# Performance work log

Measured on AMD Instinct MI355X. Metric: run time of the kernel, lower is better.

## Reference

```python
import jax, jax.numpy as jnp
import numpy as np

B, S, D, H = 2, 2048, 1024, 16
HD = D // H  # head_dim = 64
ROPE_BASE = 10000.0


def _rope_cos_sin(seq_len, head_dim, dtype=jnp.float32):
    inv_freq = 1.0 / (ROPE_BASE ** (jnp.arange(0, head_dim, 2, dtype=jnp.float32) / head_dim))
    t = jnp.arange(seq_len, dtype=jnp.float32)
    freqs = jnp.einsum('i,j->ij', t, inv_freq)          # [S, HD/2]
    emb = jnp.concatenate([freqs, freqs], axis=-1)       # [S, HD]
    return jnp.cos(emb).astype(dtype), jnp.sin(emb).astype(dtype)


def _rotate_half(x):
    x1, x2 = jnp.split(x, 2, axis=-1)
    return jnp.concatenate([-x2, x1], axis=-1)


def setup_inputs() -> dict:
    key = jax.random.key(0)
    ks = jax.random.split(key, 5)
    scale = 1.0 / np.sqrt(D)
    return {
        'hidden_states': jax.random.normal(ks[0], (B, S, D), dtype=jnp.float32),
        'Wq': jax.random.normal(ks[1], (D, D), dtype=jnp.float32) * scale,
        'Wk': jax.random.normal(ks[2], (D, D), dtype=jnp.float32) * scale,
        'Wv': jax.random.normal(ks[3], (D, D), dtype=jnp.float32) * scale,
        'Wo': jax.random.normal(ks[4], (D, D), dtype=jnp.float32) * scale,
    }


def reference(hidden_states, Wq, Wk, Wv, Wo):
    b, s, d = hidden_states.shape
    # torch nn.Linear(weight W) computes x @ W^T
    q = hidden_states @ Wq.T
    k = hidden_states @ Wk.T
    v = hidden_states @ Wv.T
    # [B, H, S, HD]
    q = q.reshape(b, s, H, HD).transpose(0, 2, 1, 3)
    k = k.reshape(b, s, H, HD).transpose(0, 2, 1, 3)
    v = v.reshape(b, s, H, HD).transpose(0, 2, 1, 3)
    cos, sin = _rope_cos_sin(s, HD, q.dtype)  # [S, HD]
    cos = cos[None, None]  # [1,1,S,HD]
    sin = sin[None, None]
    q = q * cos + _rotate_half(q) * sin
    k = k * cos + _rotate_half(k) * sin
    scale = HD ** -0.5
    attn = jnp.einsum('bhqd,bhkd->bhqk', q, k) * scale
    attn = jax.nn.softmax(attn.astype(jnp.float32), axis=-1).astype(q.dtype)
    out = jnp.einsum('bhqk,bhkd->bhqd', attn, v)
    out = out.transpose(0, 2, 1, 3).reshape(b, s, d)
    return out @ Wo.T
```

## Files before the change

kernel.cpp:

```cpp
#include <hip/hip_runtime.h>
#include <math.h>

constexpr int Bc = 2;
constexpr int Sc = 2048;
constexpr int Dc = 1024;
constexpr int Hc = 16;
constexpr int HDc = 64;

constexpr float QSC = 0.125f * 1.4426950408889634f;

typedef __attribute__((ext_vector_type(8))) short bf16x8;
typedef __attribute__((ext_vector_type(4))) float f32x4;
typedef __attribute__((ext_vector_type(4))) unsigned short us4;
typedef __attribute__((ext_vector_type(2))) unsigned int u32x2;
typedef __attribute__((ext_vector_type(4))) unsigned int u32x4;

__device__ __forceinline__ unsigned f2bf(float x) {
    unsigned u = __float_as_uint(x);
    return (u + 0x7FFFu + ((u >> 16) & 1u)) >> 16;
}

__device__ __forceinline__ void split2(float x, unsigned short& h, unsigned short& l) {
    unsigned hh = f2bf(x);
    h = (unsigned short)hh;
    l = (unsigned short)f2bf(x - __uint_as_float(hh << 16));
}

#if __has_builtin(__builtin_amdgcn_permlane32_swap)
__device__ __forceinline__ void plswap32(unsigned& a, unsigned& b) {
    u32x2 r = __builtin_amdgcn_permlane32_swap(a, b, false, false);
    a = r.x; b = r.y;
}
#else
__device__ __forceinline__ void plswap32(unsigned& a, unsigned& b) {
    asm volatile("v_permlane32_swap_b32 %0, %1" : "+v"(a), "+v"(b));
}
#endif
#if __has_builtin(__builtin_amdgcn_permlane16_swap)
__device__ __forceinline__ void plswap16(unsigned& a, unsigned& b) {
    u32x2 r = __builtin_amdgcn_permlane16_swap(a, b, false, false);
    a = r.x; b = r.y;
}
#else
__device__ __forceinline__ void plswap16(unsigned& a, unsigned& b) {
    asm volatile("v_permlane16_swap_b32 %0, %1" : "+v"(a), "+v"(b));
}
#endif

__device__ __forceinline__ void exppack(const f32x4& sv, unsigned& w0, unsigned& w1) {
    unsigned u0 = __float_as_uint(__builtin_amdgcn_exp2f(sv[0]));
    unsigned u1 = __float_as_uint(__builtin_amdgcn_exp2f(sv[1]));
    unsigned u2 = __float_as_uint(__builtin_amdgcn_exp2f(sv[2]));
    unsigned u3 = __float_as_uint(__builtin_amdgcn_exp2f(sv[3]));
    w0 = __builtin_amdgcn_perm(u1, u0, 0x07060302u);
    w1 = __builtin_amdgcn_perm(u3, u2, 0x07060302u);
}

__global__ void rope_table(float* __restrict__ ct, float* __restrict__ st_) {
    int id = blockIdx.x * 256 + threadIdx.x;
    int s = id >> 5;
    int i = id & 31;
    double invf = pow(10000.0, -(double)i / 32.0);
    double ang = (double)s * invf;
    ct[id] = (float)cos(ang);
    st_[id] = (float)sin(ang);
}

__global__ void split_xw(const float* __restrict__ x,
                         const float* __restrict__ Wq, const float* __restrict__ Wk,
                         const float* __restrict__ Wv, const float* __restrict__ Wo,
                         unsigned short* __restrict__ xh,
                         unsigned short* __restrict__ whAll, unsigned short* __restrict__ wlAll) {
    int y = blockIdx.y;
    const float* src;
    unsigned short* h;
    unsigned short* l = nullptr;
    int n;
    if (y == 0) { src = x; h = xh; n = 1 << 22; }
    else {
        src = (y == 1) ? Wq : (y == 2) ? Wk : (y == 3) ? Wv : Wo;
        h = whAll + (size_t)(y - 1) * (1 << 20);
        if (y == 4) l = wlAll + (size_t)3 * (1 << 20);
        n = 1 << 20;
    }
    int i = (blockIdx.x * 256 + threadIdx.x) * 4;
    if (i >= n) return;
    float4 v = *(const float4*)(src + i);
    us4 hh;
    ((unsigned short*)&hh)[0] = (unsigned short)f2bf(v.x);
    ((unsigned short*)&hh)[1] = (unsigned short)f2bf(v.y);
    ((unsigned short*)&hh)[2] = (unsigned short)f2bf(v.z);
    ((unsigned short*)&hh)[3] = (unsigned short)f2bf(v.w);
    *(us4*)(h + i) = hh;
    if (l) {
        us4 ll;
        const float* vp = (const float*)&v;
#pragma unroll
        for (int e = 0; e < 4; e++) {
            unsigned short hi = ((unsigned short*)&hh)[e];
            ((unsigned short*)&ll)[e] =
                (unsigned short)f2bf(vp[e] - __uint_as_float((unsigned)hi << 16));
        }
        *(us4*)(l + i) = ll;
    }
}

__global__ __launch_bounds__(512, 4) void gemm_qkv(
    const unsigned short* __restrict__ Ah,
    const unsigned short* __restrict__ whAll,
    unsigned short* __restrict__ Qh,
    unsigned short* __restrict__ Kh,
    unsigned short* __restrict__ Vh,
    const float* __restrict__ ct, const float* __restrict__ st_) {
    constexpr int K = 1024;
    __shared__ __align__(16) unsigned short As[2 * 4096], Bs[2 * 4096];

    const int z = blockIdx.z;
    const unsigned short* Wh = whAll + (size_t)z * (1 << 20);

    const int t = threadIdx.x;
    const int lane = t & 63;
    const int wave = t >> 6;
    const int l = lane & 15;
    const int quad = lane >> 4;
    const int wr = wave >> 1;
    const int wc = wave & 1;
    const int m0 = blockIdx.x * 128;
    const int n0 = blockIdx.y * 128;

    const int arow = t & 127, akc = t >> 7;
    const unsigned short* gA = Ah + (size_t)(m0 + arow) * K + akc * 8;
    const unsigned short* gB = Wh + (size_t)(n0 + arow) * K + akc * 8;

    f32x4 acc[2][4];
#pragma unroll
    for (int i = 0; i < 2; i++)
#pragma unroll
        for (int j = 0; j < 4; j++) acc[i][j] = (f32x4){0.f, 0.f, 0.f, 0.f};

    __builtin_amdgcn_global_load_lds(
        (const __attribute__((address_space(1))) unsigned int*)gA,
        (__attribute__((address_space(3))) unsigned int*)(As + t * 8), 16, 0, 0);
    __builtin_amdgcn_global_load_lds(
        (const __attribute__((address_space(1))) unsigned int*)gB,
        (__attribute__((address_space(3))) unsigned int*)(Bs + t * 8), 16, 0, 0);

    for (int it = 0; it < 32; ++it) {
        __syncthreads();
        if (it + 1 < 32) {
            const int koff = (it + 1) * 32;
            const int bo = ((it + 1) & 1) * 4096;
            __builtin_amdgcn_global_load_lds(
                (const __attribute__((address_space(1))) unsigned int*)(gA + koff),
                (__attribute__((address_space(3))) unsigned int*)(As + bo + t * 8), 16, 0, 0);
            __builtin_amdgcn_global_load_lds(
                (const __attribute__((address_space(1))) unsigned int*)(gB + koff),
                (__attribute__((address_space(3))) unsigned int*)(Bs + bo + t * 8), 16, 0, 0);
        }
        const unsigned short* a = As + (it & 1) * 4096;
        const unsigned short* bb = Bs + (it & 1) * 4096;
        bf16x8 ah[2], bh[4];
#pragma unroll
        for (int i = 0; i < 2; i++)
            ah[i] = *(const bf16x8*)&a[(quad * 128 + wr * 32 + i * 16 + l) * 8];
#pragma unroll
        for (int j = 0; j < 4; j++)
            bh[j] = *(const bf16x8*)&bb[(quad * 128 + wc * 64 + j * 16 + l) * 8];
#pragma unroll
        for (int i = 0; i < 2; i++)
#pragma unroll
            for (int j = 0; j < 4; j++)
                acc[i][j] = __builtin_amdgcn_mfma_f32_16x16x32_bf16(ah[i], bh[j], acc[i][j], 0, 0, 0);
    }

    const int hcol = blockIdx.y * 2 + wc;
    if (z == 2) {
#pragma unroll
        for (int i = 0; i < 2; i++) {
            int m_base = m0 + wr * 32 + i * 16 + quad * 4;
            int bbk = m_base >> 11;
            int T = (m_base & (Sc - 1)) >> 6;
            int ii = (2 * wr + i) & 3;
            int kk = ii >> 1;
            int qd = ((ii & 1) << 1) | (quad >> 1);
            int tj = (quad & 1) * 4;
            size_t tilebase = (((size_t)(bbk * Hc + hcol)) * 32 + T) * 4096;
#pragma unroll
            for (int jj = 0; jj < 4; jj++) {
                int d = jj * 16 + l;
                size_t off = tilebase + (size_t)(((kk * 4 + qd) * 64 + d) * 8 + tj);
                us4 v4;
#pragma unroll
                for (int r = 0; r < 4; r++)
                    ((unsigned short*)&v4)[r] = (unsigned short)f2bf(acc[i][jj][r]);
                *(us4*)(Vh + off) = v4;
            }
        }
    } else {
#pragma unroll
        for (int i = 0; i < 2; i++)
#pragma unroll
            for (int r = 0; r < 4; r++) {
                int m = m0 + wr * 32 + i * 16 + quad * 4 + r;
                int bbk = m >> 11, s = m & (Sc - 1);
#pragma unroll
                for (int jp = 0; jp < 2; jp++) {
                    int d = jp * 16 + l;
                    float cs = ct[s * 32 + d];
                    float sn = st_[s * 32 + d];
                    float x0 = acc[i][jp][r];
                    float x1 = acc[i][jp + 2][r];
                    float y0 = x0 * cs - x1 * sn;
                    float y1 = x1 * cs + x0 * sn;
                    if (z == 0) {
                        size_t rowb = (((size_t)(bbk * Hc + hcol)) * Sc + s) * HDc;
                        Qh[rowb + d]      = (unsigned short)f2bf(y0 * QSC);
                        Qh[rowb + d + 32] = (unsigned short)f2bf(y1 * QSC);
                    } else {
                        int T = s >> 6, tok = s & 63;
                        size_t tb = (((size_t)(bbk * Hc + hcol)) * 32 + T) * 8;
                        size_t off0 = ((tb + (d >> 3)) * 64 + tok) * 8 + (d & 7);
                        size_t off1 = ((tb + (d >> 3) + 4) * 64 + tok) * 8 + (d & 7);
                        Kh[off0] = (unsigned short)f2bf(y0);
                        Kh[off1] = (unsigned short)f2bf(y1);
                    }
                }
            }
    }
}

__global__ __launch_bounds__(512) void attn10(
    const unsigned short* __restrict__ Qh,
    const unsigned short* __restrict__ Kh,
    const unsigned short* __restrict__ Vh,
    unsigned short* __restrict__ AOh, unsigned short* __restrict__ AOl) {
    __shared__ __align__(16) unsigned short KsH[3 * 4096], VtH[3 * 4096];

    const int t = threadIdx.x;
    const int lane = t & 63;
    const int wave = t >> 6;
    const int l = lane & 15;
    const int quad = lane >> 4;
    const int id = blockIdx.x;
    const int bh = (id & 7) * 4 + (id >> 6);
    const int qt = (id >> 3) & 7;
    const int q0 = qt * 256;
    const int b = bh >> 4;
    const int hh = bh & 15;

    const bf16x8 ONES8 = {(short)0x3F80, (short)0x3F80, (short)0x3F80, (short)0x3F80,
                          (short)0x3F80, (short)0x3F80, (short)0x3F80, (short)0x3F80};

    bf16x8 qf[2][2];
#pragma unroll
    for (int bnd = 0; bnd < 2; bnd++) {
        size_t rowb = ((size_t)bh * Sc + q0 + wave * 32 + bnd * 16 + l) * HDc;
#pragma unroll
        for (int ks = 0; ks < 2; ks++)
            qf[bnd][ks] = *(const bf16x8*)(Qh + rowb + ks * 32 + quad * 8);
    }

    f32x4 o[2][4], lac[2];
#pragma unroll
    for (int bnd = 0; bnd < 2; bnd++) {
        lac[bnd] = (f32x4){0.f, 0.f, 0.f, 0.f};
#pragma unroll
        for (int i = 0; i < 4; i++) o[bnd][i] = (f32x4){0.f, 0.f, 0.f, 0.f};
    }

    const int tensor = wave >> 2;
    const int coff0 = (wave * 2) & 7;
    unsigned short* larr = tensor ? VtH : KsH;
    const unsigned short* gT =
        (tensor ? Vh : Kh) + (size_t)bh * Sc * HDc + coff0 * 512 + lane * 8;

#pragma unroll
    for (int q = 0; q < 2; q++)
        __builtin_amdgcn_global_load_lds(
            (const __attribute__((address_space(1))) unsigned int*)(gT + q * 512),
            (__attribute__((address_space(3))) unsigned int*)(larr + coff0 * 512 + q * 512),
            16, 0, 0);

    int bc = 0;
    for (int kt = 0; kt < 32; kt++) {
        if (kt + 1 < 32) {
            int nb = bc + 1; if (nb == 3) nb = 0;
            const unsigned short* g = gT + (size_t)(kt + 1) * 4096;
            unsigned short* dst = larr + nb * 4096 + coff0 * 512;
#pragma unroll
            for (int q = 0; q < 2; q++)
                __builtin_amdgcn_global_load_lds(
                    (const __attribute__((address_space(1))) unsigned int*)(g + q * 512),
                    (__attribute__((address_space(3))) unsigned int*)(dst + q * 512),
                    16, 0, 0);
            asm volatile("s_waitcnt vmcnt(2)" ::: "memory");
        } else {
            asm volatile("s_waitcnt vmcnt(0)" ::: "memory");
        }
        __builtin_amdgcn_s_barrier();
        const unsigned short* Kbuf = KsH + bc * 4096;
        const unsigned short* Vbuf = VtH + bc * 4096;

        f32x4 s[2][4];
#pragma unroll
        for (int bnd = 0; bnd < 2; bnd++)
#pragma unroll
            for (int tt = 0; tt < 4; tt++) s[bnd][tt] = (f32x4){0.f, 0.f, 0.f, 0.f};
        __builtin_amdgcn_s_setprio(1);
#pragma unroll
        for (int ks = 0; ks < 2; ks++)
#pragma unroll
            for (int tt = 0; tt < 4; tt++) {
                bf16x8 kf = *(const bf16x8*)&Kbuf[((ks * 4 + quad) * 64 + tt * 16 + l) * 8];
                s[0][tt] = __builtin_amdgcn_mfma_f32_16x16x32_bf16(kf, qf[0][ks], s[0][tt], 0, 0, 0);
                s[1][tt] = __builtin_amdgcn_mfma_f32_16x16x32_bf16(kf, qf[1][ks], s[1][tt], 0, 0, 0);
            }
        __builtin_amdgcn_s_setprio(0);

        bf16x8 pf[2][2];
#pragma unroll
        for (int bnd = 0; bnd < 2; bnd++)
#pragma unroll
            for (int ttp = 0; ttp < 2; ttp++) {
                unsigned A0, A1, B0, B1;
                exppack(s[bnd][2 * ttp], A0, A1);
                exppack(s[bnd][2 * ttp + 1], B0, B1);
                plswap32(A0, B0);
                plswap16(A0, B0);
                plswap32(A1, B1);
                plswap16(A1, B1);
                u32x4 fw = {A0, A1, B0, B1};
                bf16x8 p8 = __builtin_bit_cast(bf16x8, fw);
                pf[bnd][ttp] = p8;
                lac[bnd] = __builtin_amdgcn_mfma_f32_16x16x32_bf16(ONES8, p8, lac[bnd], 0, 0, 0);
            }

        __builtin_amdgcn_s_setprio(1);
#pragma unroll
        for (int kk = 0; kk < 2; kk++)
#pragma unroll
            for (int dd = 0; dd < 4; dd++) {
                bf16x8 vf = *(const bf16x8*)
                    &Vbuf[(size_t)((kk * 4 + quad) * 64 + dd * 16 + l) * 8];
                o[0][dd] = __builtin_amdgcn_mfma_f32_16x16x32_bf16(vf, pf[0][kk], o[0][dd], 0, 0, 0);
                o[1][dd] = __builtin_amdgcn_mfma_f32_16x16x32_bf16(vf, pf[1][kk], o[1][dd], 0, 0, 0);
            }
        __builtin_amdgcn_s_setprio(0);
        if (++bc == 3) bc = 0;
    }

#pragma unroll
    for (int bnd = 0; bnd < 2; bnd++) {
        float inv = 1.f / lac[bnd][0];
        int q = q0 + wave * 32 + bnd * 16 + l;
        size_t rowb = ((size_t)b * Sc + q) * Dc + hh * HDc + quad * 4;
#pragma unroll
        for (int dd = 0; dd < 4; dd++) {
            us4 h4, l4;
#pragma unroll
            for (int r = 0; r < 4; r++)
                split2(o[bnd][dd][r] * inv,
                       ((unsigned short*)&h4)[r], ((unsigned short*)&l4)[r]);
            *(us4*)(AOh + rowb + dd * 16) = h4;
            *(us4*)(AOl + rowb + dd * 16) = l4;
        }
    }
}

__global__ __launch_bounds__(512, 4) void gemm_out(
    const unsigned short* __restrict__ Ah, const unsigned short* __restrict__ Al,
    const unsigned short* __restrict__ Wh, const unsigned short* __restrict__ Wl,
    float* __restrict__ C0, float* __restrict__ C1) {
    constexpr int K = 1024;
    __shared__ __align__(16) unsigned short AsH[2 * 4096], AsL[2 * 4096],
                                            BsH[2 * 4096], BsL[2 * 4096];

    const int t = threadIdx.x;
    const int lane = t & 63;
    const int wave = t >> 6;
    const int l = lane & 15;
    const int quad = lane >> 4;
    const int wr = wave >> 1;
    const int wc = wave & 1;
    const int m0 = blockIdx.x * 128;
    const int n0 = blockIdx.y * 128;
    const int k0 = blockIdx.z * 512;
    float* __restrict__ C = blockIdx.z ? C1 : C0;

    const int arow = t & 127, akc = t >> 7;
    const unsigned short* gah = Ah + (size_t)(m0 + arow) * K + k0 + akc * 8;
    const unsigned short* gal = Al + (size_t)(m0 + arow) * K + k0 + akc * 8;
    const unsigned short* gbh = Wh + (size_t)(n0 + arow) * K + k0 + akc * 8;
    const unsigned short* gbl = Wl + (size_t)(n0 + arow) * K + k0 + akc * 8;

    f32x4 acc[2][4];
#pragma unroll
    for (int i = 0; i < 2; i++)
#pragma unroll
        for (int j = 0; j < 4; j++) acc[i][j] = (f32x4){0.f, 0.f, 0.f, 0.f};

#define STAGE_OUT(koff, bo)                                                                \
    do {                                                                                   \
        __builtin_amdgcn_global_load_lds(                                                  \
            (const __attribute__((address_space(1))) unsigned int*)(gah + (koff)),         \
            (__attribute__((address_space(3))) unsigned int*)(AsH + (bo) + t * 8), 16, 0, 0); \
        __builtin_amdgcn_global_load_lds(                                                  \
            (const __attribute__((address_space(1))) unsigned int*)(gal + (koff)),         \
            (__attribute__((address_space(3))) unsigned int*)(AsL + (bo) + t * 8), 16, 0, 0); \
        __builtin_amdgcn_global_load_lds(                                                  \
            (const __attribute__((address_space(1))) unsigned int*)(gbh + (koff)),         \
            (__attribute__((address_space(3))) unsigned int*)(BsH + (bo) + t * 8), 16, 0, 0); \
        __builtin_amdgcn_global_load_lds(                                                  \
            (const __attribute__((address_space(1))) unsigned int*)(gbl + (koff)),         \
            (__attribute__((address_space(3))) unsigned int*)(BsL + (bo) + t * 8), 16, 0, 0); \
    } while (0)

    STAGE_OUT(0, 0);

    for (int it = 0; it < 16; ++it) {
        __syncthreads();
        if (it + 1 < 16) STAGE_OUT((it + 1) * 32, ((it + 1) & 1) * 4096);
        const int bo = (it & 1) * 4096;
        bf16x8 ah[2], al[2], bh[4], bl[4];
#pragma unroll
        for (int i = 0; i < 2; i++) {
            int ra = bo + (quad * 128 + wr * 32 + i * 16 + l) * 8;
            ah[i] = *(const bf16x8*)&AsH[ra];
            al[i] = *(const bf16x8*)&AsL[ra];
        }
#pragma unroll
        for (int j = 0; j < 4; j++) {
            int rb = bo + (quad * 128 + wc * 64 + j * 16 + l) * 8;
            bh[j] = *(const bf16x8*)&BsH[rb];
            bl[j] = *(const bf16x8*)&BsL[rb];
        }
#pragma unroll
        for (int i = 0; i < 2; i++)
#pragma unroll
            for (int j = 0; j < 4; j++) {
                acc[i][j] = __builtin_amdgcn_mfma_f32_16x16x32_bf16(ah[i], bh[j], acc[i][j], 0, 0, 0);
                acc[i][j] = __builtin_amdgcn_mfma_f32_16x16x32_bf16(al[i], bh[j], acc[i][j], 0, 0, 0);
                acc[i][j] = __builtin_amdgcn_mfma_f32_16x16x32_bf16(ah[i], bl[j], acc[i][j], 0, 0, 0);
            }
    }
#undef STAGE_OUT

#pragma unroll
    for (int i = 0; i < 2; i++)
#pragma unroll
        for (int j = 0; j < 4; j++)
#pragma unroll
            for (int r = 0; r < 4; r++) {
                int m = m0 + wr * 32 + i * 16 + quad * 4 + r;
                int n = n0 + wc * 64 + j * 16 + l;
                C[(size_t)m * Dc + n] = acc[i][j][r];
            }
}

__global__ void add_partial(float* __restrict__ out, const float* __restrict__ p1) {
    int i = (blockIdx.x * 256 + threadIdx.x) * 4;
    float4 a = *(const float4*)(out + i);
    float4 b = *(const float4*)(p1 + i);
    a.x += b.x; a.y += b.y; a.z += b.z; a.w += b.w;
    *(float4*)(out + i) = a;
}

extern "C" void kernel_launch(void* const* d_in, const int* in_sizes, int n_in,
                              void* d_out, int out_size, void* d_ws, size_t ws_size,
                              hipStream_t stream) {
    const float* x  = (const float*)d_in[0];
    const float* Wq = (const float*)d_in[1];
    const float* Wk = (const float*)d_in[2];
    const float* Wv = (const float*)d_in[3];
    const float* Wo = (const float*)d_in[4];
    float* out = (float*)d_out;

    unsigned short* usw = (unsigned short*)d_ws;
    const size_t M4 = (size_t)1 << 22;
    unsigned short* whAll = usw;
    unsigned short* wlAll = usw + M4;
    unsigned short* xh = usw + 2 * M4;
    unsigned short* xl = usw + 3 * M4;
    unsigned short* Qh = usw + 4 * M4;
    unsigned short* Kh = usw + 5 * M4;
    unsigned short* Vh = usw + 6 * M4;
    float* ct = (float*)(usw + 7 * M4);
    float* st_ = ct + (size_t)Sc * 32;
    unsigned short* AOh = xh;
    unsigned short* AOl = xl;
    float* P1 = (float*)Qh;

    rope_table<<<dim3((Sc * 32) / 256), dim3(256), 0, stream>>>(ct, st_);
    split_xw<<<dim3(4096, 5), dim3(256), 0, stream>>>(x, Wq, Wk, Wv, Wo, xh, whAll, wlAll);
    gemm_qkv<<<dim3(32, 8, 3), dim3(512), 0, stream>>>(
        xh, whAll, Qh, Kh, Vh, ct, st_);
    attn10<<<dim3(256), dim3(512), 0, stream>>>(Qh, Kh, Vh, AOh, AOl);
    gemm_out<<<dim3(32, 8, 2), dim3(512), 0, stream>>>(
        AOh, AOl, whAll + 3 * (1 << 20), wlAll + 3 * (1 << 20), out, P1);
    add_partial<<<dim3(4096), dim3(256), 0, stream>>>(out, P1);
}
```

Baseline: 229.4 us.

## Enlarge QKV GEMM tiles to 256x256 with finer-grained staged pipeline

Result: slower. 241.7 us (+5.4%).

```diff
diff --git a/kernel.cpp b/kernel.cpp
--- a/kernel.cpp
+++ b/kernel.cpp
@@ -14,6 +14,9 @@
 typedef __attribute__((ext_vector_type(4))) unsigned short us4;
 typedef __attribute__((ext_vector_type(2))) unsigned int u32x2;
 typedef __attribute__((ext_vector_type(4))) unsigned int u32x4;
+
+typedef const __attribute__((address_space(1))) unsigned int* gp_t;
+typedef __attribute__((address_space(3))) unsigned int* lp_t;
 
 __device__ __forceinline__ unsigned f2bf(float x) {
     unsigned u = __float_as_uint(x);
@@ -105,7 +108,7 @@
     }
 }
 
-__global__ __launch_bounds__(512, 4) void gemm_qkv(
+__global__ __launch_bounds__(512, 2) void gemm_qkv8(
     const unsigned short* __restrict__ Ah,
     const unsigned short* __restrict__ whAll,
     unsigned short* __restrict__ Qh,
@@ -113,81 +116,122 @@
     unsigned short* __restrict__ Vh,
     const float* __restrict__ ct, const float* __restrict__ st_) {
     constexpr int K = 1024;
-    __shared__ __align__(16) unsigned short As[2 * 4096], Bs[2 * 4096];
-
-    const int z = blockIdx.z;
-    const unsigned short* Wh = whAll + (size_t)z * (1 << 20);
+    __shared__ __align__(16) unsigned short As[2][16384], Bs[2][16384];
 
     const int t = threadIdx.x;
     const int lane = t & 63;
     const int wave = t >> 6;
-    const int l = lane & 15;
+    const int l15 = lane & 15;
     const int quad = lane >> 4;
-    const int wr = wave >> 1;
-    const int wc = wave & 1;
-    const int m0 = blockIdx.x * 128;
-    const int n0 = blockIdx.y * 128;
-
-    const int arow = t & 127, akc = t >> 7;
-    const unsigned short* gA = Ah + (size_t)(m0 + arow) * K + akc * 8;
-    const unsigned short* gB = Wh + (size_t)(n0 + arow) * K + akc * 8;
-
-    f32x4 acc[2][4];
-#pragma unroll
-    for (int i = 0; i < 2; i++)
+    const int wr = wave >> 2;
+    const int wc = wave & 3;
+    const int m0 = blockIdx.x * 256;
+    const int n0 = blockIdx.y * 256;
+    const int z = blockIdx.z;
+    const unsigned short* Wh = whAll + (size_t)z * (1 << 20);
+
+    const int kcr0 = (2 * wave + 0) >> 2, rb0 = ((2 * wave + 0) & 3) * 64;
+    const int kcr1 = (2 * wave + 1) >> 2, rb1 = ((2 * wave + 1) & 3) * 64;
+    const unsigned short* gA0 = Ah + (size_t)(m0 + rb0 + lane) * K + kcr0 * 8;
+    const unsigned short* gA1 = Ah + (size_t)(m0 + rb1 + lane) * K + kcr1 * 8;
+    const unsigned short* gB0 = Wh + (size_t)(n0 + rb0 + lane) * K + kcr0 * 8;
+    const unsigned short* gB1 = Wh + (size_t)(n0 + rb1 + lane) * K + kcr1 * 8;
+    const int ld0 = (kcr0 * 256 + rb0 + lane) * 8;
+    const int ld1 = (kcr1 * 256 + rb1 + lane) * 8;
+
+    f32x4 acc[8][4];
+#pragma unroll
+    for (int i = 0; i < 8; i++)
 #pragma unroll
         for (int j = 0; j < 4; j++) acc[i][j] = (f32x4){0.f, 0.f, 0.f, 0.f};
-
-    __builtin_amdgcn_global_load_lds(
-        (const __attribute__((address_space(1))) unsigned int*)gA,
-        (__attribute__((address_space(3))) unsigned int*)(As + t * 8), 16, 0, 0);
-    __builtin_amdgcn_global_load_lds(
-        (const __attribute__((address_space(1))) unsigned int*)gB,
-        (__attribute__((address_space(3))) unsigned int*)(Bs + t * 8), 16, 0, 0);
-
-    for (int it = 0; it < 32; ++it) {
-        __syncthreads();
-        if (it + 1 < 32) {
-            const int koff = (it + 1) * 32;
-            const int bo = ((it + 1) & 1) * 4096;
-            __builtin_amdgcn_global_load_lds(
-                (const __attribute__((address_space(1))) unsigned int*)(gA + koff),
-                (__attribute__((address_space(3))) unsigned int*)(As + bo + t * 8), 16, 0, 0);
-            __builtin_amdgcn_global_load_lds(
-                (const __attribute__((address_space(1))) unsigned int*)(gB + koff),
-                (__attribute__((address_space(3))) unsigned int*)(Bs + bo + t * 8), 16, 0, 0);
-        }
-        const unsigned short* a = As + (it & 1) * 4096;
-        const unsigned short* bb = Bs + (it & 1) * 4096;
-        bf16x8 ah[2], bh[4];
-#pragma unroll
-        for (int i = 0; i < 2; i++)
-            ah[i] = *(const bf16x8*)&a[(quad * 128 + wr * 32 + i * 16 + l) * 8];
-#pragma unroll
-        for (int j = 0; j < 4; j++)
-            bh[j] = *(const bf16x8*)&bb[(quad * 128 + wc * 64 + j * 16 + l) * 8];
-#pragma unroll
-        for (int i = 0; i < 2; i++)
-#pragma unroll
-            for (int j = 0; j < 4; j++)
-                acc[i][j] = __builtin_amdgcn_mfma_f32_16x16x32_bf16(ah[i], bh[j], acc[i][j], 0, 0, 0);
-    }
-
-    const int hcol = blockIdx.y * 2 + wc;
+    bf16x8 af[8];
+
+#define STG(g0, g1, LARR, X, KH) do {                                                      \
+        const int _ko = (X) * 64 + (KH) * 32;                                              \
+        const int _lo = (KH) * 8192;                                                       \
+        __builtin_amdgcn_global_load_lds((gp_t)((g0) + _ko),                               \
+            (lp_t)(&LARR[(X) & 1][ld0 + _lo]), 16, 0, 0);                                  \
+        __builtin_amdgcn_global_load_lds((gp_t)((g1) + _ko),                               \
+            (lp_t)(&LARR[(X) & 1][ld1 + _lo]), 16, 0, 0);                                  \
+    } while (0)
+
+#define VM10 asm volatile("s_waitcnt vmcnt(10)" ::: "memory")
+#define VM8  asm volatile("s_waitcnt vmcnt(8)" ::: "memory")
+#define VM4  asm volatile("s_waitcnt vmcnt(4)" ::: "memory")
+#define VM0  asm volatile("s_waitcnt vmcnt(0)" ::: "memory")
+
+#define CPH(BUF, KS, J0, RA, PRE) do {                                                     \
+        PRE;                                                                               \
+        asm volatile("s_barrier" ::: "memory");                                            \
+        const unsigned short* _a = &As[(BUF)][0];                                          \
+        const unsigned short* _b = &Bs[(BUF)][0];                                          \
+        if (RA) {                                                                          \
+            _Pragma("unroll")                                                              \
+            for (int _i = 0; _i < 8; _i++)                                                 \
+                af[_i] = *(const bf16x8*)&_a[((KS) * 4 + quad) * 2048 +                    \
+                                             (wr * 128 + _i * 16 + l15) * 8];              \
+        }                                                                                  \
+        bf16x8 _bf0 = *(const bf16x8*)&_b[((KS) * 4 + quad) * 2048 +                       \
+                                          (wc * 64 + (J0) * 16 + l15) * 8];                \
+        bf16x8 _bf1 = *(const bf16x8*)&_b[((KS) * 4 + quad) * 2048 +                       \
+                                          (wc * 64 + ((J0) + 1) * 16 + l15) * 8];          \
+        __builtin_amdgcn_s_setprio(1);                                                     \
+        _Pragma("unroll")                                                                  \
+        for (int _i = 0; _i < 8; _i++) {                                                   \
+            acc[_i][(J0)]     = __builtin_amdgcn_mfma_f32_16x16x32_bf16(af[_i], _bf0,      \
+                                    acc[_i][(J0)], 0, 0, 0);                               \
+            acc[_i][(J0) + 1] = __builtin_amdgcn_mfma_f32_16x16x32_bf16(af[_i], _bf1,      \
+                                    acc[_i][(J0) + 1], 0, 0, 0);                           \
+        }                                                                                  \
+        __builtin_amdgcn_s_setprio(0);                                                     \
+        asm volatile("s_barrier" ::: "memory");                                            \
+    } while (0)
+
+    STG(gA0, gA1, As, 0, 0); STG(gB0, gB1, Bs, 0, 0);
+    STG(gA0, gA1, As, 0, 1); STG(gB0, gB1, Bs, 0, 1);
+    STG(gA0, gA1, As, 1, 0); STG(gB0, gB1, Bs, 1, 0);
+
+    for (int e = 0; e < 14; e += 2) {
+        CPH(0, 0, 0, 1, STG(gA0, gA1, As, e + 1, 1); VM10);
+        CPH(0, 0, 2, 0, STG(gB0, gB1, Bs, e + 1, 1));
+        CPH(0, 1, 0, 1, STG(gA0, gA1, As, e + 2, 0); VM10);
+        CPH(0, 1, 2, 0, STG(gB0, gB1, Bs, e + 2, 0));
+        CPH(1, 0, 0, 1, STG(gA0, gA1, As, e + 2, 1); VM10);
+        CPH(1, 0, 2, 0, STG(gB0, gB1, Bs, e + 2, 1));
+        CPH(1, 1, 0, 1, STG(gA0, gA1, As, e + 3, 0); VM10);
+        CPH(1, 1, 2, 0, STG(gB0, gB1, Bs, e + 3, 0));
+    }
+    CPH(0, 0, 0, 1, STG(gA0, gA1, As, 15, 1); VM10);
+    CPH(0, 0, 2, 0, STG(gB0, gB1, Bs, 15, 1));
+    CPH(0, 1, 0, 1, VM8);
+    CPH(0, 1, 2, 0, );
+    CPH(1, 0, 0, 1, VM4);
+    CPH(1, 0, 2, 0, );
+    CPH(1, 1, 0, 1, VM0);
+    CPH(1, 1, 2, 0, );
+
+#undef CPH
+#undef STG
+#undef VM10
+#undef VM8
+#undef VM4
+#undef VM0
+
+    const int hcol = blockIdx.y * 4 + wc;
     if (z == 2) {
 #pragma unroll
-        for (int i = 0; i < 2; i++) {
-            int m_base = m0 + wr * 32 + i * 16 + quad * 4;
+        for (int i = 0; i < 8; i++) {
+            int m_base = m0 + wr * 128 + i * 16 + quad * 4;
             int bbk = m_base >> 11;
             int T = (m_base & (Sc - 1)) >> 6;
-            int ii = (2 * wr + i) & 3;
+            int ii = i & 3;
             int kk = ii >> 1;
             int qd = ((ii & 1) << 1) | (quad >> 1);
             int tj = (quad & 1) * 4;
             size_t tilebase = (((size_t)(bbk * Hc + hcol)) * 32 + T) * 4096;
 #pragma unroll
             for (int jj = 0; jj < 4; jj++) {
-                int d = jj * 16 + l;
+                int d = jj * 16 + l15;
                 size_t off = tilebase + (size_t)(((kk * 4 + qd) * 64 + d) * 8 + tj);
                 us4 v4;
 #pragma unroll
@@ -198,14 +242,14 @@
         }
     } else {
 #pragma unroll
-        for (int i = 0; i < 2; i++)
+        for (int i = 0; i < 8; i++)
 #pragma unroll
             for (int r = 0; r < 4; r++) {
-                int m = m0 + wr * 32 + i * 16 + quad * 4 + r;
+                int m = m0 + wr * 128 + i * 16 + quad * 4 + r;
                 int bbk = m >> 11, s = m & (Sc - 1);
 #pragma unroll
                 for (int jp = 0; jp < 2; jp++) {
-                    int d = jp * 16 + l;
+                    int d = jp * 16 + l15;
                     float cs = ct[s * 32 + d];
                     float sn = st_[s * 32 + d];
                     float x0 = acc[i][jp][r];
@@ -277,8 +321,8 @@
 #pragma unroll
     for (int q = 0; q < 2; q++)
         __builtin_amdgcn_global_load_lds(
-            (const __attribute__((address_space(1))) unsigned int*)(gT + q * 512),
-            (__attribute__((address_space(3))) unsigned int*)(larr + coff0 * 512 + q * 512),
+            (gp_t)(gT + q * 512),
+            (lp_t)(larr + coff0 * 512 + q * 512),
             16, 0, 0);
 
     int bc = 0;
@@ -290,8 +334,8 @@
 #pragma unroll
             for (int q = 0; q < 2; q++)
                 __builtin_amdgcn_global_load_lds(
-                    (const __attribute__((address_space(1))) unsigned int*)(g + q * 512),
-                    (__attribute__((address_space(3))) unsigned int*)(dst + q * 512),
+                    (gp_t)(g + q * 512),
+                    (lp_t)(dst + q * 512),
                     16, 0, 0);
             asm volatile("s_waitcnt vmcnt(2)" ::: "memory");
         } else {
@@ -401,18 +445,14 @@
 
 #define STAGE_OUT(koff, bo)                                                                \
     do {                                                                                   \
-        __builtin_amdgcn_global_load_lds(                                                  \
-            (const __attribute__((address_space(1))) unsigned int*)(gah + (koff)),         \
-            (__attribute__((address_space(3))) unsigned int*)(AsH + (bo) + t * 8), 16, 0, 0); \
-        __builtin_amdgcn_global_load_lds(                                                  \
-            (const __attribute__((address_space(1))) unsigned int*)(gal + (koff)),         \
-            (__attribute__((address_space(3))) unsigned int*)(AsL + (bo) + t * 8), 16, 0, 0); \
-        __builtin_amdgcn_global_load_lds(                                                  \
-            (const __attribute__((address_space(1))) unsigned int*)(gbh + (koff)),         \
-            (__attribute__((address_space(3))) unsigned int*)(BsH + (bo) + t * 8), 16, 0, 0); \
-        __builtin_amdgcn_global_load_lds(                                                  \
-            (const __attribute__((address_space(1))) unsigned int*)(gbl + (koff)),         \
-            (__attribute__((address_space(3))) unsigned int*)(BsL + (bo) + t * 8), 16, 0, 0); \
+        __builtin_amdgcn_global_load_lds((gp_t)(gah + (koff)),                             \
+            (lp_t)(AsH + (bo) + t * 8), 16, 0, 0);                                         \
+        __builtin_amdgcn_global_load_lds((gp_t)(gal + (koff)),                             \
+            (lp_t)(AsL + (bo) + t * 8), 16, 0, 0);                                         \
+        __builtin_amdgcn_global_load_lds((gp_t)(gbh + (koff)),                             \
+            (lp_t)(BsH + (bo) + t * 8), 16, 0, 0);                                         \
+        __builtin_amdgcn_global_load_lds((gp_t)(gbl + (koff)),                             \
+            (lp_t)(BsL + (bo) + t * 8), 16, 0, 0);                                         \
     } while (0)
 
     STAGE_OUT(0, 0);
@@ -492,7 +532,7 @@
 
     rope_table<<<dim3((Sc * 32) / 256), dim3(256), 0, stream>>>(ct, st_);
     split_xw<<<dim3(4096, 5), dim3(256), 0, stream>>>(x, Wq, Wk, Wv, Wo, xh, whAll, wlAll);
-    gemm_qkv<<<dim3(32, 8, 3), dim3(512), 0, stream>>>(
+    gemm_qkv8<<<dim3(16, 4, 3), dim3(512), 0, stream>>>(
         xh, whAll, Qh, Kh, Vh, ct, st_);
     attn10<<<dim3(256), dim3(512), 0, stream>>>(Qh, Kh, Vh, AOh, AOl);
     gemm_out<<<dim3(32, 8, 2), dim3(512), 0, stream>>>(
```

## Use row-major XOR-swizzled LDS tiles and K=64 stages in QKV and output GEMMs

Applied to the files above, without the earlier changes.

Result: faster. 203.4 us (-11.4%).

```diff
diff --git a/kernel.cpp b/kernel.cpp
--- a/kernel.cpp
+++ b/kernel.cpp
@@ -14,6 +14,9 @@
 typedef __attribute__((ext_vector_type(4))) unsigned short us4;
 typedef __attribute__((ext_vector_type(2))) unsigned int u32x2;
 typedef __attribute__((ext_vector_type(4))) unsigned int u32x4;
+
+typedef const __attribute__((address_space(1))) unsigned int* gp_t;
+typedef __attribute__((address_space(3))) unsigned int* lp_t;
 
 __device__ __forceinline__ unsigned f2bf(float x) {
     unsigned u = __float_as_uint(x);
@@ -105,7 +108,7 @@
     }
 }
 
-__global__ __launch_bounds__(512, 4) void gemm_qkv(
+__global__ __launch_bounds__(512, 4) void gemm_qkv9(
     const unsigned short* __restrict__ Ah,
     const unsigned short* __restrict__ whAll,
     unsigned short* __restrict__ Qh,
@@ -113,24 +116,27 @@
     unsigned short* __restrict__ Vh,
     const float* __restrict__ ct, const float* __restrict__ st_) {
     constexpr int K = 1024;
-    __shared__ __align__(16) unsigned short As[2 * 4096], Bs[2 * 4096];
-
-    const int z = blockIdx.z;
-    const unsigned short* Wh = whAll + (size_t)z * (1 << 20);
+    __shared__ __align__(16) unsigned short As[2][8192], Bs[2][8192];
 
     const int t = threadIdx.x;
     const int lane = t & 63;
     const int wave = t >> 6;
-    const int l = lane & 15;
+    const int l15 = lane & 15;
     const int quad = lane >> 4;
     const int wr = wave >> 1;
     const int wc = wave & 1;
     const int m0 = blockIdx.x * 128;
     const int n0 = blockIdx.y * 128;
-
-    const int arow = t & 127, akc = t >> 7;
-    const unsigned short* gA = Ah + (size_t)(m0 + arow) * K + akc * 8;
-    const unsigned short* gB = Wh + (size_t)(n0 + arow) * K + akc * 8;
+    const int z = blockIdx.z;
+    const unsigned short* Wh = whAll + (size_t)z * (1 << 20);
+
+    const int c0 = t,        r0 = c0 >> 3, s0 = c0 & 7;
+    const int c1 = t + 512,  r1 = c1 >> 3, s1 = c1 & 7;
+    const unsigned short* gA0 = Ah + (size_t)(m0 + r0) * K + (s0 ^ (r0 & 7)) * 8;
+    const unsigned short* gA1 = Ah + (size_t)(m0 + r1) * K + (s1 ^ (r1 & 7)) * 8;
+    const unsigned short* gB0 = Wh + (size_t)(n0 + r0) * K + (s0 ^ (r0 & 7)) * 8;
+    const unsigned short* gB1 = Wh + (size_t)(n0 + r1) * K + (s1 ^ (r1 & 7)) * 8;
+    const int d0 = c0 * 8, d1 = c1 * 8;
 
     f32x4 acc[2][4];
 #pragma unroll
@@ -138,40 +144,43 @@
 #pragma unroll
         for (int j = 0; j < 4; j++) acc[i][j] = (f32x4){0.f, 0.f, 0.f, 0.f};
 
-    __builtin_amdgcn_global_load_lds(
-        (const __attribute__((address_space(1))) unsigned int*)gA,
-        (__attribute__((address_space(3))) unsigned int*)(As + t * 8), 16, 0, 0);
-    __builtin_amdgcn_global_load_lds(
-        (const __attribute__((address_space(1))) unsigned int*)gB,
-        (__attribute__((address_space(3))) unsigned int*)(Bs + t * 8), 16, 0, 0);
-
-    for (int it = 0; it < 32; ++it) {
+#define STGQ(X) do {                                                                       \
+        const int _ko = (X) * 64;                                                          \
+        const int _bf = (X) & 1;                                                           \
+        __builtin_amdgcn_global_load_lds((gp_t)(gA0 + _ko), (lp_t)(&As[_bf][d0]), 16, 0, 0); \
+        __builtin_amdgcn_global_load_lds((gp_t)(gA1 + _ko), (lp_t)(&As[_bf][d1]), 16, 0, 0); \
+        __builtin_amdgcn_global_load_lds((gp_t)(gB0 + _ko), (lp_t)(&Bs[_bf][d0]), 16, 0, 0); \
+        __builtin_amdgcn_global_load_lds((gp_t)(gB1 + _ko), (lp_t)(&Bs[_bf][d1]), 16, 0, 0); \
+    } while (0)
+
+    STGQ(0);
+
+    for (int it = 0; it < 16; ++it) {
         __syncthreads();
-        if (it + 1 < 32) {
-            const int koff = (it + 1) * 32;
-            const int bo = ((it + 1) & 1) * 4096;
-            __builtin_amdgcn_global_load_lds(
-                (const __attribute__((address_space(1))) unsigned int*)(gA + koff),
-                (__attribute__((address_space(3))) unsigned int*)(As + bo + t * 8), 16, 0, 0);
-            __builtin_amdgcn_global_load_lds(
-                (const __attribute__((address_space(1))) unsigned int*)(gB + koff),
-                (__attribute__((address_space(3))) unsigned int*)(Bs + bo + t * 8), 16, 0, 0);
-        }
-        const unsigned short* a = As + (it & 1) * 4096;
-        const unsigned short* bb = Bs + (it & 1) * 4096;
-        bf16x8 ah[2], bh[4];
-#pragma unroll
-        for (int i = 0; i < 2; i++)
-            ah[i] = *(const bf16x8*)&a[(quad * 128 + wr * 32 + i * 16 + l) * 8];
-#pragma unroll
-        for (int j = 0; j < 4; j++)
-            bh[j] = *(const bf16x8*)&bb[(quad * 128 + wc * 64 + j * 16 + l) * 8];
-#pragma unroll
-        for (int i = 0; i < 2; i++)
-#pragma unroll
-            for (int j = 0; j < 4; j++)
-                acc[i][j] = __builtin_amdgcn_mfma_f32_16x16x32_bf16(ah[i], bh[j], acc[i][j], 0, 0, 0);
-    }
+        if (it + 1 < 16) STGQ(it + 1);
+        const unsigned short* a = &As[it & 1][0];
+        const unsigned short* bb = &Bs[it & 1][0];
+#pragma unroll
+        for (int ks = 0; ks < 2; ks++) {
+            bf16x8 ah[2], bh[4];
+#pragma unroll
+            for (int i = 0; i < 2; i++) {
+                int row = wr * 32 + i * 16 + l15;
+                ah[i] = *(const bf16x8*)&a[row * 64 + ((ks * 4 + quad) ^ (row & 7)) * 8];
+            }
+#pragma unroll
+            for (int j = 0; j < 4; j++) {
+                int row = wc * 64 + j * 16 + l15;
+                bh[j] = *(const bf16x8*)&bb[row * 64 + ((ks * 4 + quad) ^ (row & 7)) * 8];
+            }
+#pragma unroll
+            for (int i = 0; i < 2; i++)
+#pragma unroll
+                for (int j = 0; j < 4; j++)
+                    acc[i][j] = __builtin_amdgcn_mfma_f32_16x16x32_bf16(ah[i], bh[j], acc[i][j], 0, 0, 0);
+        }
+    }
+#undef STGQ
 
     const int hcol = blockIdx.y * 2 + wc;
     if (z == 2) {
@@ -187,7 +196,7 @@
             size_t tilebase = (((size_t)(bbk * Hc + hcol)) * 32 + T) * 4096;
 #pragma unroll
             for (int jj = 0; jj < 4; jj++) {
-                int d = jj * 16 + l;
+                int d = jj * 16 + l15;
                 size_t off = tilebase + (size_t)(((kk * 4 + qd) * 64 + d) * 8 + tj);
                 us4 v4;
 #pragma unroll
@@ -205,7 +214,7 @@
                 int bbk = m >> 11, s = m & (Sc - 1);
 #pragma unroll
                 for (int jp = 0; jp < 2; jp++) {
-                    int d = jp * 16 + l;
+                    int d = jp * 16 + l15;
                     float cs = ct[s * 32 + d];
                     float sn = st_[s * 32 + d];
                     float x0 = acc[i][jp][r];
@@ -277,8 +286,8 @@
 #pragma unroll
     for (int q = 0; q < 2; q++)
         __builtin_amdgcn_global_load_lds(
-            (const __attribute__((address_space(1))) unsigned int*)(gT + q * 512),
-            (__attribute__((address_space(3))) unsigned int*)(larr + coff0 * 512 + q * 512),
+            (gp_t)(gT + q * 512),
+            (lp_t)(larr + coff0 * 512 + q * 512),
             16, 0, 0);
 
     int bc = 0;
@@ -290,8 +299,8 @@
 #pragma unroll
             for (int q = 0; q < 2; q++)
                 __builtin_amdgcn_global_load_lds(
-                    (const __attribute__((address_space(1))) unsigned int*)(g + q * 512),
-                    (__attribute__((address_space(3))) unsigned int*)(dst + q * 512),
+                    (gp_t)(g + q * 512),
+                    (lp_t)(dst + q * 512),
                     16, 0, 0);
             asm volatile("s_waitcnt vmcnt(2)" ::: "memory");
         } else {
@@ -367,18 +376,18 @@
     }
 }
 
-__global__ __launch_bounds__(512, 4) void gemm_out(
+__global__ __launch_bounds__(512, 4) void gemm_out9(
     const unsigned short* __restrict__ Ah, const unsigned short* __restrict__ Al,
     const unsigned short* __restrict__ Wh, const unsigned short* __restrict__ Wl,
     float* __restrict__ C0, float* __restrict__ C1) {
     constexpr int K = 1024;
-    __shared__ __align__(16) unsigned short AsH[2 * 4096], AsL[2 * 4096],
-                                            BsH[2 * 4096], BsL[2 * 4096];
+    __shared__ __align__(16) unsigned short AsH[2][4096], AsL[2][4096],
+                                            BsH[2][4096], BsL[2][4096];
 
     const int t = threadIdx.x;
     const int lane = t & 63;
     const int wave = t >> 6;
-    const int l = lane & 15;
+    const int l15 = lane & 15;
     const int quad = lane >> 4;
     const int wr = wave >> 1;
     const int wc = wave & 1;
@@ -387,11 +396,13 @@
     const int k0 = blockIdx.z * 512;
     float* __restrict__ C = blockIdx.z ? C1 : C0;
 
-    const int arow = t & 127, akc = t >> 7;
-    const unsigned short* gah = Ah + (size_t)(m0 + arow) * K + k0 + akc * 8;
-    const unsigned short* gal = Al + (size_t)(m0 + arow) * K + k0 + akc * 8;
-    const unsigned short* gbh = Wh + (size_t)(n0 + arow) * K + k0 + akc * 8;
-    const unsigned short* gbl = Wl + (size_t)(n0 + arow) * K + k0 + akc * 8;
+    const int rr = t >> 2, ss = t & 3;
+    const int gc = (ss ^ (rr & 3)) * 8;
+    const unsigned short* gah = Ah + (size_t)(m0 + rr) * K + k0 + gc;
+    const unsigned short* gal = Al + (size_t)(m0 + rr) * K + k0 + gc;
+    const unsigned short* gbh = Wh + (size_t)(n0 + rr) * K + k0 + gc;
+    const unsigned short* gbl = Wl + (size_t)(n0 + rr) * K + k0 + gc;
+    const int dd_ = t * 8;
 
     f32x4 acc[2][4];
 #pragma unroll
@@ -399,40 +410,35 @@
 #pragma unroll
         for (int j = 0; j < 4; j++) acc[i][j] = (f32x4){0.f, 0.f, 0.f, 0.f};
 
-#define STAGE_OUT(koff, bo)                                                                \
-    do {                                                                                   \
-        __builtin_amdgcn_global_load_lds(                                                  \
-            (const __attribute__((address_space(1))) unsigned int*)(gah + (koff)),         \
-            (__attribute__((address_space(3))) unsigned int*)(AsH + (bo) + t * 8), 16, 0, 0); \
-        __builtin_amdgcn_global_load_lds(                                                  \
-            (const __attribute__((address_space(1))) unsigned int*)(gal + (koff)),         \
-            (__attribute__((address_space(3))) unsigned int*)(AsL + (bo) + t * 8), 16, 0, 0); \
-        __builtin_amdgcn_global_load_lds(                                                  \
-            (const __attribute__((address_space(1))) unsigned int*)(gbh + (koff)),         \
-            (__attribute__((address_space(3))) unsigned int*)(BsH + (bo) + t * 8), 16, 0, 0); \
-        __builtin_amdgcn_global_load_lds(                                                  \
-            (const __attribute__((address_space(1))) unsigned int*)(gbl + (koff)),         \
-            (__attribute__((address_space(3))) unsigned int*)(BsL + (bo) + t * 8), 16, 0, 0); \
+#define STGO(X) do {                                                                       \
+        const int _ko = (X) * 32;                                                          \
+        const int _bf = (X) & 1;                                                           \
+        __builtin_amdgcn_global_load_lds((gp_t)(gah + _ko), (lp_t)(&AsH[_bf][dd_]), 16, 0, 0); \
+        __builtin_amdgcn_global_load_lds((gp_t)(gal + _ko), (lp_t)(&AsL[_bf][dd_]), 16, 0, 0); \
+        __builtin_amdgcn_global_load_lds((gp_t)(gbh + _ko), (lp_t)(&BsH[_bf][dd_]), 16, 0, 0); \
+        __builtin_amdgcn_global_load_lds((gp_t)(gbl + _ko), (lp_t)(&BsL[_bf][dd_]), 16, 0, 0); \
     } while (0)
 
-    STAGE_OUT(0, 0);
+    STGO(0);
 
     for (int it = 0; it < 16; ++it) {
         __syncthreads();
-        if (it + 1 < 16) STAGE_OUT((it + 1) * 32, ((it + 1) & 1) * 4096);
-        const int bo = (it & 1) * 4096;
+        if (it + 1 < 16) STGO(it + 1);
+        const int bf = it & 1;
         bf16x8 ah[2], al[2], bh[4], bl[4];
 #pragma unroll
         for (int i = 0; i < 2; i++) {
-            int ra = bo + (quad * 128 + wr * 32 + i * 16 + l) * 8;
-            ah[i] = *(const bf16x8*)&AsH[ra];
-            al[i] = *(const bf16x8*)&AsL[ra];
+            int row = wr * 32 + i * 16 + l15;
+            int ra = row * 32 + (quad ^ (row & 3)) * 8;
+            ah[i] = *(const bf16x8*)&AsH[bf][ra];
+            al[i] = *(const bf16x8*)&AsL[bf][ra];
         }
 #pragma unroll
         for (int j = 0; j < 4; j++) {
-            int rb = bo + (quad * 128 + wc * 64 + j * 16 + l) * 8;
-            bh[j] = *(const bf16x8*)&BsH[rb];
-            bl[j] = *(const bf16x8*)&BsL[rb];
+            int row = wc * 64 + j * 16 + l15;
+            int rb = row * 32 + (quad ^ (row & 3)) * 8;
+            bh[j] = *(const bf16x8*)&BsH[bf][rb];
+            bl[j] = *(const bf16x8*)&BsL[bf][rb];
         }
 #pragma unroll
         for (int i = 0; i < 2; i++)
@@ -443,7 +449,7 @@
                 acc[i][j] = __builtin_amdgcn_mfma_f32_16x16x32_bf16(ah[i], bl[j], acc[i][j], 0, 0, 0);
             }
     }
-#undef STAGE_OUT
+#undef STGO
 
 #pragma unroll
     for (int i = 0; i < 2; i++)
@@ -452,7 +458,7 @@
 #pragma unroll
             for (int r = 0; r < 4; r++) {
                 int m = m0 + wr * 32 + i * 16 + quad * 4 + r;
-                int n = n0 + wc * 64 + j * 16 + l;
+                int n = n0 + wc * 64 + j * 16 + l15;
                 C[(size_t)m * Dc + n] = acc[i][j][r];
             }
 }
@@ -492,10 +498,10 @@
 
     rope_table<<<dim3((Sc * 32) / 256), dim3(256), 0, stream>>>(ct, st_);
     split_xw<<<dim3(4096, 5), dim3(256), 0, stream>>>(x, Wq, Wk, Wv, Wo, xh, whAll, wlAll);
-    gemm_qkv<<<dim3(32, 8, 3), dim3(512), 0, stream>>>(
+    gemm_qkv9<<<dim3(32, 8, 3), dim3(512), 0, stream>>>(
         xh, whAll, Qh, Kh, Vh, ct, st_);
     attn10<<<dim3(256), dim3(512), 0, stream>>>(Qh, Kh, Vh, AOh, AOl);
-    gemm_out<<<dim3(32, 8, 2), dim3(512), 0, stream>>>(
+    gemm_out9<<<dim3(32, 8, 2), dim3(512), 0, stream>>>(
         AOh, AOl, whAll + 3 * (1 << 20), wlAll + 3 * (1 << 20), out, P1);
     add_partial<<<dim3(4096), dim3(256), 0, stream>>>(out, P1);
 }
```
